# Performance work log

Hardware: AMD Instinct MI355X
Metric: run time of the kernel (lower is better)

Reference implementation:

```python
import jax, jax.numpy as jnp
import numpy as np

NUM_HEADS = 8
D_MODEL = 512
HEAD_DIM = D_MODEL // NUM_HEADS


def _conv1x1(x, W, b):
    # Conv1d(kernel_size=1): x [B, Cin, N], W [Cout, Cin], b [Cout] -> [B, Cout, N]
    return jnp.einsum('oi,bin->bon', W, x) + b[None, :, None]


def setup_inputs() -> dict:
    key = jax.random.key(0)
    ks = jax.random.split(key, 12)
    B, D, N, Mlen = 4, D_MODEL, 2048, 2048
    inp = {
        'query': jax.random.normal(ks[0], (B, D, N), dtype=jnp.float32),
        'key':   jax.random.normal(ks[1], (B, D, Mlen), dtype=jnp.float32),
        'value': jax.random.normal(ks[2], (B, D, Mlen), dtype=jnp.float32),
        'M':     jnp.ones((B, N, Mlen), dtype=jnp.int32),
    }
    scale = 0.02
    inp['Wq'] = jax.random.normal(ks[3], (D, D), dtype=jnp.float32) * scale
    inp['bq'] = jnp.zeros((D,), dtype=jnp.float32)
    inp['Wk'] = jax.random.normal(ks[4], (D, D), dtype=jnp.float32) * scale
    inp['bk'] = jnp.zeros((D,), dtype=jnp.float32)
    inp['Wv'] = jax.random.normal(ks[5], (D, D), dtype=jnp.float32) * scale
    inp['bv'] = jnp.zeros((D,), dtype=jnp.float32)
    inp['Wm'] = jax.random.normal(ks[6], (D, D), dtype=jnp.float32) * scale
    inp['bm'] = jnp.zeros((D,), dtype=jnp.float32)
    return inp


def reference(query, key, value, M, Wq, bq, Wk, bk, Wv, bv, Wm, bm):
    B = query.shape[0]
    # 1x1-conv projections, then channel split as [head_dim, heads] (matches torch .view)
    q = _conv1x1(query, Wq, bq).reshape(B, HEAD_DIM, NUM_HEADS, -1)  # [B, d, h, N]
    k = _conv1x1(key,   Wk, bk).reshape(B, HEAD_DIM, NUM_HEADS, -1)  # [B, d, h, M]
    v = _conv1x1(value, Wv, bv).reshape(B, HEAD_DIM, NUM_HEADS, -1)  # [B, d, h, M]
    scores = jnp.einsum('bdhn,bdhm->bhnm', q, k) / jnp.sqrt(jnp.float32(HEAD_DIM))
    # mask: positions with M==0 are disallowed -> fill with -finfo.max
    bad = (1 - M)[:, None, :, :].astype(bool)  # [B, 1, N, M], broadcasts over heads
    scores = jnp.where(bad, -jnp.finfo(scores.dtype).max, scores)
    prob = jax.nn.softmax(scores, axis=-1)  # [B, h, N, M]
    x = jnp.einsum('bhnm,bdhm->bdhn', prob, v)  # [B, d, h, N]
    out = _conv1x1(x.reshape(B, HEAD_DIM * NUM_HEADS, -1), Wm, bm)  # [B, D, N]
    return out
```

## Files before the change

kernel.cpp:

```cpp
#include <hip/hip_runtime.h>

typedef __attribute__((ext_vector_type(8))) short s8v;
typedef __attribute__((ext_vector_type(4))) float f4v;
typedef _Float16 h8 __attribute__((ext_vector_type(8)));
typedef unsigned short u16;
typedef unsigned long long u64;

#define DM 512
#define NH 8
#define HD 64
#define BB 4
#define NN 2048

extern "C" __device__ float __ocml_native_exp2_f32(float);
__device__ __forceinline__ float fexp2(float x){ return __ocml_native_exp2_f32(x); }

__device__ __forceinline__ float bf2f(u16 x){ return __uint_as_float(((unsigned)x)<<16); }
__device__ __forceinline__ u16 f2bf(float f){
  unsigned u = __float_as_uint(f);
  u += 0x7FFFu + ((u>>16)&1u);
  return (u16)(u>>16);
}
__device__ __forceinline__ void gl2lds16(const u16* g, u16* l){
  __builtin_amdgcn_global_load_lds((__attribute__((address_space(1))) void*)(g),
                                   (__attribute__((address_space(3))) void*)(l), 16, 0, 0);
}

__global__ __launch_bounds__(256) void k_maskpack(const int* M, u64* bits){
  int tid = threadIdx.x;
  int wv = tid>>6, lane = tid&63;
  size_t w0 = (size_t)blockIdx.x*64 + wv*16;
  #pragma unroll
  for (int it=0; it<16; it++){
    int v = M[(w0+it)*64 + lane];
    u64 bal = __ballot(v == 1);
    if (lane == 0) bits[w0+it] = bal;
  }
}

__global__ void k_prep(const float* Wq, const float* bq, const float* Wk, const float* bk,
                       const float* Wv, const float* bv, const float* Wm,
                       u16* Wp, u16* Wmp, float* bp,
                       const u64* bits, u64* allw){
  int blk = blockIdx.x, tid = threadIdx.x;
  if (blk < 1536){
    int t = blk >> 9, op = blk & 511;
    int srow = ((op & 63) << 3) | (op >> 6);
    const float* W = (t==0) ? Wq : ((t==1) ? Wk : Wv);
    for (int j = tid; j < 512; j += 256)
      Wp[((size_t)t*512 + op)*512 + j] = f2bf(W[(size_t)srow*512 + j]);
  } else if (blk < 2048){
    int o = blk - 1536;
    for (int c = tid; c < 512; c += 256){
      int scol = ((c & 63) << 3) | (c >> 6);
      Wmp[(size_t)o*512 + c] = f2bf(Wm[(size_t)o*512 + scol]);
    }
  } else if (blk == 2048){
    for (int idx = tid; idx < 1536; idx += 256){
      int t = idx >> 9, op = idx & 511;
      const float* bs = (t==0) ? bq : ((t==1) ? bk : bv);
      int srow = ((op & 63) << 3) | (op >> 6);
      bp[idx] = bs[srow];
    }
  } else {
    __shared__ u64 red[256];
    int bnt = blk - 2049;
    int mt = tid & 31, rg = tid >> 5;
    const u64* base = bits + (size_t)bnt*64*32;
    u64 v = ~0ull;
    #pragma unroll
    for (int j=0;j<8;j++) v &= base[(size_t)(rg*8+j)*32 + mt];
    red[tid] = v;
    __syncthreads();
    if (tid < 32){
      u64 a = red[tid];
      #pragma unroll
      for (int g2=1; g2<8; g2++) a &= red[g2*32 + tid];
      allw[(size_t)bnt*32 + tid] = a;
    }
  }
}

__global__ __launch_bounds__(256) void k_transpose(const float* q, const float* k, const float* v, u16* XT){
  __shared__ u16 T[64*72];
  int blk = blockIdx.x, tid = threadIdx.x;
  int rt = blk & 31; blk >>= 5;
  int it = blk & 7;  blk >>= 3;
  int b  = blk & 3;  int t = blk >> 2;
  const float* src = (t==0) ? q : ((t==1) ? k : v);
  src += (size_t)b*DM*NN;
  int i0 = it*64, r0 = rt*64;
  int il = tid>>4, rj = (tid&15)*4;
  #pragma unroll
  for (int p=0;p<4;p++){
    int i = il + p*16;
    float4 vv = *(const float4*)&src[(size_t)(i0+i)*NN + r0 + rj];
    float fv[4] = {vv.x, vv.y, vv.z, vv.w};
    #pragma unroll
    for (int qq=0;qq<4;qq++){
      int r = rj + qq;
      int sr = ((r&3)<<4) | (r>>2);
      T[sr*72 + i] = f2bf(fv[qq]);
    }
  }
  __syncthreads();
  u16* dst = XT + ((size_t)(t*4+b)*NN)*DM;
  int rl = tid>>3, ib = (tid&7)*8;
  #pragma unroll
  for (int p=0;p<2;p++){
    int r = rl + p*32;
    int sr = ((r&3)<<4) | (r>>2);
    s8v vv = *(s8v*)&T[sr*72 + ib];
    *(s8v*)&dst[(size_t)(r0+r)*DM + i0 + ib] = vv;
  }
}

__global__ __launch_bounds__(256) void k_proj(const u16* XT, const u16* Wp, const float* bp,
                                              u16* P, u16* VT){
  __shared__ u16 Al[128*32];
  __shared__ u16 Bl[128*32];
  __shared__ u16 S[128*72];
  int blk = blockIdx.x, tid = threadIdx.x;
  int nt = blk / 192; int mt = blk % 192;
  int tb = mt >> 4;
  int t  = tb >> 2, b = tb & 3;
  int r0 = (mt & 15)*128, o0 = nt*128;
  const u16* Abase = XT + ((size_t)tb*NN + r0)*DM;
  const u16* Bbase = Wp + ((size_t)t*512 + o0)*DM;

  int w = tid>>6, L = tid&63, li = L&15, lq = L>>4;
  int wr = w>>1, wc = w&1;
  int srow = tid>>2;
  int g8   = ((tid&3) ^ ((tid>>3)&3))*8;
  u16* AldsW = &Al[((tid&192))*8];
  u16* BldsW = &Bl[((tid&192))*8];
  int sw = (li>>1)&3;

  f4v acc[4][4];
  #pragma unroll
  for (int a=0;a<4;a++)
    #pragma unroll
    for (int c2=0;c2<4;c2++) acc[a][c2] = (f4v){0.f,0.f,0.f,0.f};

  for (int kk=0; kk<16; kk++){
    int k0 = kk*32;
    __syncthreads();
    #pragma unroll
    for (int c=0;c<2;c++){
      gl2lds16(&Abase[(size_t)(srow + c*64)*DM + k0 + g8], AldsW + c*2048);
      gl2lds16(&Bbase[(size_t)(srow + c*64)*DM + k0 + g8], BldsW + c*2048);
    }
    __syncthreads();
    s8v af[4], bfr[4];
    #pragma unroll
    for (int a=0;a<4;a++){
      int r = wr*64 + a*16 + li;
      af[a] = *(s8v*)&Al[r*32 + ((lq ^ sw))*8];
    }
    #pragma unroll
    for (int c2=0;c2<4;c2++){
      int r = wc*64 + c2*16 + li;
      bfr[c2] = *(s8v*)&Bl[r*32 + ((lq ^ sw))*8];
    }
    #pragma unroll
    for (int a=0;a<4;a++)
      #pragma unroll
      for (int c2=0;c2<4;c2++)
        acc[a][c2] = __builtin_amdgcn_mfma_f32_16x16x32_bf16(af[a], bfr[c2], acc[a][c2], 0, 0, 0);
  }

  if (t < 2){
    float scale = (t==0) ? 0.18033688f : 1.0f;
    #pragma unroll
    for (int p=0;p<2;p++){
      if (wc == p){
        #pragma unroll
        for (int c2=0;c2<4;c2++){
          int cl = c2*16 + li;
          float bias = bp[t*512 + o0 + p*64 + cl];
          #pragma unroll
          for (int a=0;a<4;a++)
            #pragma unroll
            for (int ri=0;ri<4;ri++)
              S[(wr*64 + a*16 + lq*4 + ri)*72 + cl] = f2bf((acc[a][c2][ri] + bias)*scale);
        }
      }
      __syncthreads();
      int row = tid>>1, cb = (tid&1)*32;
      int hh = (o0>>6) + p;
      u16* Pb = P + (((size_t)tb*NH + hh)*NN + r0 + row)*HD + cb;
      #pragma unroll
      for (int c=0;c<4;c++){
        s8v vv = *(s8v*)&S[row*72 + cb + c*8];
        *(s8v*)&Pb[c*8] = vv;
      }
      __syncthreads();
    }
  } else {
    int mp = mt & 15;
    #pragma unroll
    for (int p=0;p<2;p++){
      if (wc == p){
        #pragma unroll
        for (int c2=0;c2<4;c2++){
          int cl = c2*16 + li;
          float bias = bp[2*512 + o0 + p*64 + cl];
          #pragma unroll
          for (int a=0;a<4;a++)
            #pragma unroll
            for (int ri=0;ri<4;ri++){
              _Float16 hh = (_Float16)(acc[a][c2][ri] + bias);
              S[(wr*64 + a*16 + lq*4 + ri)*72 + cl] = *(const u16*)&hh;
            }
        }
      }
      __syncthreads();
      int hh = (o0>>6) + p;
      u16* Vbw = VT + ((size_t)(b*NH + hh)*16 + mp)*8192;
      #pragma unroll
      for (int it2=0; it2<4; it2++){
        int c = tid + it2*256;
        int w2  = c >> 8;
        int d   = (c >> 2) & 63;
        int lq2 = c & 3;
        u16 tmp[8];
        #pragma unroll
        for (int t2=0;t2<8;t2++){
          int ml = ((t2>>2)<<6) + w2*16 + lq2*4 + (t2&3);
          tmp[t2] = S[ml*72 + d];
        }
        *(s8v*)&Vbw[(size_t)w2*2048 + d*32 + lq2*8] = *(s8v*)&tmp[0];
      }
      __syncthreads();
    }
  }
}

__global__ __launch_bounds__(256) void k_flash(const u16* Pq, const u16* VT, const u64* bits,
                                               const u64* allw, u16* Xout){
  __shared__ __align__(16) char smem[18432 + 1024];
  float* Red = (float*)smem;
  float* lsb = (float*)(smem + 18432);

  int blk = blockIdx.x, tid = threadIdx.x;
  int bh = blk & 31; int nt = blk >> 5;
  int b = bh >> 3;
  int n0 = nt*64;
  const size_t TSZ = (size_t)BB*NH*NN*HD;
  const u16* Qb = Pq + ((size_t)bh*NN + n0)*HD;
  const u16* Kb = Pq + TSZ + (size_t)bh*NN*HD;
  const u16* Vb = VT + (size_t)bh*NN*HD;
  const u64* awp = allw + ((size_t)b*32 + nt)*32;

  int w = tid>>6, L = tid&63, li = L&15, lq = L>>4;

  s8v Qf[4][2];
  #pragma unroll
  for (int j=0;j<4;j++)
    #pragma unroll
    for (int h2=0;h2<2;h2++)
      Qf[j][h2] = *(const s8v*)&Qb[(size_t)(j*16+li)*HD + h2*32 + lq*8];

  f4v O[4][4];
  #pragma unroll
  for (int j2=0;j2<4;j2++)
    #pragma unroll
    for (int j=0;j<4;j++) O[j2][j] = (f4v){0.f,0.f,0.f,0.f};
  float ls[4] = {0.f,0.f,0.f,0.f};

  const u16* Krow = Kb + (size_t)(w*16 + li)*HD + lq*8;
  const u16* Vrow = Vb + (size_t)w*2048 + li*32 + lq*8;

  s8v cKA0 = *(const s8v*)&Krow[0];
  s8v cKA1 = *(const s8v*)&Krow[32];
  s8v cKB0 = *(const s8v*)&Krow[4096];
  s8v cKB1 = *(const s8v*)&Krow[4128];

  int mbit = w*16 + lq*4;

  for (int mp=0; mp<16; mp++){
    size_t noff = (size_t)((mp+1)&15)*8192;
    s8v nKA0 = *(const s8v*)&Krow[noff];
    s8v nKA1 = *(const s8v*)&Krow[noff + 32];
    s8v nKB0 = *(const s8v*)&Krow[noff + 4096];
    s8v nKB1 = *(const s8v*)&Krow[noff + 4128];
    size_t voff = (size_t)mp*8192;
    h8 cV[4];
    #pragma unroll
    for (int j2=0;j2<4;j2++) cV[j2] = *(const h8*)&Vrow[voff + j2*512];

    u64 awA = awp[2*mp], awB = awp[2*mp+1];
    h8 Pf[4];
    f4v S[4];

    __builtin_amdgcn_s_setprio(1);
    #pragma unroll
    for (int j=0;j<4;j++){
      f4v c = (f4v){0.f,0.f,0.f,0.f};
      c = __builtin_amdgcn_mfma_f32_16x16x32_bf16(cKA0, Qf[j][0], c, 0, 0, 0);
      c = __builtin_amdgcn_mfma_f32_16x16x32_bf16(cKA1, Qf[j][1], c, 0, 0, 0);
      S[j] = c;
    }
    __builtin_amdgcn_s_setprio(0);
    if (awA == ~0ull){
      #pragma unroll
      for (int j=0;j<4;j++){
        float e0 = fexp2(S[j][0]), e1 = fexp2(S[j][1]);
        float e2 = fexp2(S[j][2]), e3 = fexp2(S[j][3]);
        ls[j] += (e0+e1)+(e2+e3);
        Pf[j][0] = (_Float16)e0; Pf[j][1] = (_Float16)e1;
        Pf[j][2] = (_Float16)e2; Pf[j][3] = (_Float16)e3;
      }
    } else {
      #pragma unroll
      for (int j=0;j<4;j++){
        u64 mw = bits[((size_t)b*NN + n0 + j*16 + li)*32 + 2*mp];
        float e[4];
        #pragma unroll
        for (int r=0;r<4;r++){
          float ev = fexp2(S[j][r]);
          e[r] = ((mw>>(mbit+r)) & 1ull) ? ev : 0.f;
          Pf[j][r] = (_Float16)e[r];
        }
        ls[j] += (e[0]+e[1])+(e[2]+e[3]);
      }
    }

    __builtin_amdgcn_s_setprio(1);
    #pragma unroll
    for (int j=0;j<4;j++){
      f4v c = (f4v){0.f,0.f,0.f,0.f};
      c = __builtin_amdgcn_mfma_f32_16x16x32_bf16(cKB0, Qf[j][0], c, 0, 0, 0);
      c = __builtin_amdgcn_mfma_f32_16x16x32_bf16(cKB1, Qf[j][1], c, 0, 0, 0);
      S[j] = c;
    }
    __builtin_amdgcn_s_setprio(0);
    if (awB == ~0ull){
      #pragma unroll
      for (int j=0;j<4;j++){
        float e0 = fexp2(S[j][0]), e1 = fexp2(S[j][1]);
        float e2 = fexp2(S[j][2]), e3 = fexp2(S[j][3]);
        ls[j] += (e0+e1)+(e2+e3);
        Pf[j][4] = (_Float16)e0; Pf[j][5] = (_Float16)e1;
        Pf[j][6] = (_Float16)e2; Pf[j][7] = (_Float16)e3;
      }
    } else {
      #pragma unroll
      for (int j=0;j<4;j++){
        u64 mw = bits[((size_t)b*NN + n0 + j*16 + li)*32 + 2*mp + 1];
        float e[4];
        #pragma unroll
        for (int r=0;r<4;r++){
          float ev = fexp2(S[j][r]);
          e[r] = ((mw>>(mbit+r)) & 1ull) ? ev : 0.f;
          Pf[j][4+r] = (_Float16)e[r];
        }
        ls[j] += (e[0]+e[1])+(e[2]+e[3]);
      }
    }

    __builtin_amdgcn_s_setprio(1);
    #pragma unroll
    for (int j2=0;j2<4;j2++)
      #pragma unroll
      for (int j=0;j<4;j++)
        O[j2][j] = __builtin_amdgcn_mfma_f32_16x16x32_f16(cV[j2], Pf[j], O[j2][j], 0, 0, 0);
    __builtin_amdgcn_s_setprio(0);

    cKA0 = nKA0; cKA1 = nKA1; cKB0 = nKB0; cKB1 = nKB1;
  }

  #pragma unroll
  for (int j=0;j<4;j++){
    float r = ls[j];
    r += __shfl_xor(r, 16); r += __shfl_xor(r, 32);
    ls[j] = r;
  }
  if (lq == 0){
    #pragma unroll
    for (int j=0;j<4;j++) lsb[w*64 + j*16 + li] = ls[j];
  }
  __syncthreads();

  #pragma unroll
  for (int ph=0; ph<4; ph++){
    if (w == ph){
      #pragma unroll
      for (int j=0;j<4;j++)
        #pragma unroll
        for (int j2=0;j2<4;j2++){
          f4v* p = (f4v*)&Red[(j*16+li)*68 + j2*16 + lq*4];
          if (ph == 0) *p = O[j2][j];
          else { f4v t = *p; t += O[j2][j]; *p = t; }
        }
    }
    __syncthreads();
  }

  int n = tid>>2, d0 = (tid&3)*16;
  float s = lsb[n] + lsb[64+n] + lsb[128+n] + lsb[192+n];
  float inv = (s > 0.f) ? 1.0f/s : 0.f;
  int h = bh & 7;
  u16* Xo = Xout + ((size_t)b*NN + n0 + n)*DM + h*HD + d0;
  u16 tmp[16];
  #pragma unroll
  for (int e2=0;e2<4;e2++){
    f4v vv = *(f4v*)&Red[n*68 + d0 + e2*4];
    #pragma unroll
    for (int q2=0;q2<4;q2++) tmp[e2*4+q2] = f2bf(vv[q2]*inv);
  }
  *(s8v*)&Xo[0] = *(s8v*)&tmp[0];
  *(s8v*)&Xo[8] = *(s8v*)&tmp[8];
}

__global__ __launch_bounds__(256) void k_out(const u16* Wmp, const u16* Xout, const float* bm, float* out){
  __shared__ u16 Al[64*32];
  __shared__ u16 Bl[128*32];
  int blk = blockIdx.x, tid = threadIdx.x;
  int nt = blk & 15; blk >>= 4;
  int ot = blk & 7;  int b = blk >> 3;
  int o0 = ot*64, n0 = nt*128;
  const u16* Abase = Wmp + (size_t)o0*DM;
  const u16* Bbase = Xout + ((size_t)b*NN + n0)*DM;

  int w = tid>>6, L = tid&63, li = L&15, lq = L>>4;
  int wo = w&1, wn = w>>1;
  int srow = tid>>2;
  int g8   = ((tid&3) ^ ((tid>>3)&3))*8;
  u16* AldsW = &Al[((tid&192))*8];
  u16* BldsW = &Bl[((tid&192))*8];
  int sw = (li>>1)&3;

  f4v acc[2][4];
  #pragma unroll
  for (int a=0;a<2;a++)
    #pragma unroll
    for (int c2=0;c2<4;c2++) acc[a][c2] = (f4v){0.f,0.f,0.f,0.f};

  for (int kk=0; kk<16; kk++){
    int k0 = kk*32;
    __syncthreads();
    gl2lds16(&Abase[(size_t)srow*DM + k0 + g8], AldsW);
    #pragma unroll
    for (int c=0;c<2;c++)
      gl2lds16(&Bbase[(size_t)(srow + c*64)*DM + k0 + g8], BldsW + c*2048);
    __syncthreads();
    s8v af[2], bfr[4];
    #pragma unroll
    for (int a=0;a<2;a++){
      int r = wo*32 + a*16 + li;
      af[a] = *(s8v*)&Al[r*32 + ((lq ^ sw))*8];
    }
    #pragma unroll
    for (int c2=0;c2<4;c2++){
      int r = wn*64 + c2*16 + li;
      bfr[c2] = *(s8v*)&Bl[r*32 + ((lq ^ sw))*8];
    }
    #pragma unroll
    for (int a=0;a<2;a++)
      #pragma unroll
      for (int c2=0;c2<4;c2++)
        acc[a][c2] = __builtin_amdgcn_mfma_f32_16x16x32_bf16(af[a], bfr[c2], acc[a][c2], 0, 0, 0);
  }

  #pragma unroll
  for (int a=0;a<2;a++){
    #pragma unroll
    for (int ri=0;ri<4;ri++){
      int o = o0 + wo*32 + a*16 + lq*4 + ri;
      float bias = bm[o];
      float* ob = out + ((size_t)b*DM + o)*NN + n0 + wn*64;
      #pragma unroll
      for (int c2=0;c2<4;c2++)
        ob[c2*16 + li] = acc[a][c2][ri] + bias;
    }
  }
}

extern "C" void kernel_launch(void* const* d_in, const int* in_sizes, int n_in,
                              void* d_out, int out_size, void* d_ws, size_t ws_size,
                              hipStream_t stream){
  const float* q  = (const float*)d_in[0];
  const float* k  = (const float*)d_in[1];
  const float* v  = (const float*)d_in[2];
  const int*   M  = (const int*)d_in[3];
  const float* Wq = (const float*)d_in[4];
  const float* bq = (const float*)d_in[5];
  const float* Wk = (const float*)d_in[6];
  const float* bk = (const float*)d_in[7];
  const float* Wv = (const float*)d_in[8];
  const float* bv = (const float*)d_in[9];
  const float* Wm = (const float*)d_in[10];
  const float* bm = (const float*)d_in[11];

  char* ws = (char*)d_ws;
  u16*   XT   = (u16*)(ws + 0);
  u16*   P    = (u16*)(ws + 25165824);
  u16*   VT   = (u16*)(ws + 41943040);
  u16*   Wp   = (u16*)(ws + 50331648);
  u16*   Wmp  = (u16*)(ws + 51904512);
  float* bp   = (float*)(ws + 52428800);
  u64*   bits = (u64*)(ws + 52434944);
  u16*   Xout = (u16*)(ws + 54532096);
  u64*   allw = (u64*)(ws + 62920704);
  float* out  = (float*)d_out;

  k_maskpack<<<4096, 256, 0, stream>>>(M, bits);
  k_prep<<<2177, 256, 0, stream>>>(Wq, bq, Wk, bk, Wv, bv, Wm, Wp, Wmp, bp, bits, allw);
  k_transpose<<<3072, 256, 0, stream>>>(q, k, v, XT);
  k_proj<<<768, 256, 0, stream>>>(XT, Wp, bp, P, VT);
  k_flash<<<1024, 256, 0, stream>>>(P, VT, bits, allw, Xout);
  k_out<<<512, 256, 0, stream>>>(Wmp, Xout, bm, out);
}
```

Measured before the change: 278.2 us.

## Fuse mask packing, weight prep and transpose into one pre kernel; trim flash registers

Merges the mask-packing, weight/bias prep and input-transpose kernels into a single launch. The mask-block AND reduction is now computed directly from the ballots, so the separate pass over the bits buffer goes away and two launches are saved. In the flash kernel, the cross-iteration K prefetch is removed, the V load moves after the first QK MFMA, and launch bounds request 3 blocks per SM to lower register pressure and raise occupancy. The cost is less explicit latency hiding of the K loads.

```diff
diff --git a/kernel.cpp b/kernel.cpp
--- a/kernel.cpp
+++ b/kernel.cpp
@@ -26,36 +26,55 @@
                                    (__attribute__((address_space(3))) void*)(l), 16, 0, 0);
 }
 
-__global__ __launch_bounds__(256) void k_maskpack(const int* M, u64* bits){
-  int tid = threadIdx.x;
-  int wv = tid>>6, lane = tid&63;
-  size_t w0 = (size_t)blockIdx.x*64 + wv*16;
-  #pragma unroll
-  for (int it=0; it<16; it++){
-    int v = M[(w0+it)*64 + lane];
-    u64 bal = __ballot(v == 1);
-    if (lane == 0) bits[w0+it] = bal;
-  }
-}
-
-__global__ void k_prep(const float* Wq, const float* bq, const float* Wk, const float* bk,
+__global__ __launch_bounds__(256) void k_pre(const int* M, u64* bits, u64* allw,
+                       const float* Wq, const float* bq, const float* Wk, const float* bk,
                        const float* Wv, const float* bv, const float* Wm,
                        u16* Wp, u16* Wmp, float* bp,
-                       const u64* bits, u64* allw){
+                       const float* q, const float* k, const float* v, u16* XT){
+  __shared__ u16 T[64*72];
+  __shared__ u64 red[4][8];
   int blk = blockIdx.x, tid = threadIdx.x;
-  if (blk < 1536){
-    int t = blk >> 9, op = blk & 511;
+
+  if (blk < 512){
+    int mg = blk & 3, bnt = blk >> 2;
+    int wv = tid>>6, lane = tid&63;
+    const int* Mb = M + (size_t)bnt*64*2048 + (size_t)mg*512;
+    u64 acc[8];
+    #pragma unroll
+    for (int j=0;j<8;j++) acc[j] = ~0ull;
+    for (int rr=0; rr<16; rr++){
+      int row = wv*16 + rr;
+      #pragma unroll
+      for (int j=0;j<8;j++){
+        int vv = Mb[(size_t)row*2048 + j*64 + lane];
+        u64 bal = __ballot(vv == 1);
+        acc[j] &= bal;
+        if (lane == 0) bits[((size_t)bnt*64 + row)*32 + mg*8 + j] = bal;
+      }
+    }
+    if (lane == 0){
+      #pragma unroll
+      for (int j=0;j<8;j++) red[wv][j] = acc[j];
+    }
+    __syncthreads();
+    if (tid < 8){
+      u64 a = red[0][tid] & red[1][tid] & red[2][tid] & red[3][tid];
+      allw[(size_t)bnt*32 + mg*8 + tid] = a;
+    }
+  } else if (blk < 2048){
+    int idx = blk - 512;
+    int t = idx >> 9, op = idx & 511;
     int srow = ((op & 63) << 3) | (op >> 6);
     const float* W = (t==0) ? Wq : ((t==1) ? Wk : Wv);
     for (int j = tid; j < 512; j += 256)
       Wp[((size_t)t*512 + op)*512 + j] = f2bf(W[(size_t)srow*512 + j]);
-  } else if (blk < 2048){
-    int o = blk - 1536;
+  } else if (blk < 2560){
+    int o = blk - 2048;
     for (int c = tid; c < 512; c += 256){
       int scol = ((c & 63) << 3) | (c >> 6);
       Wmp[(size_t)o*512 + c] = f2bf(Wm[(size_t)o*512 + scol]);
     }
-  } else if (blk == 2048){
+  } else if (blk == 2560){
     for (int idx = tid; idx < 1536; idx += 256){
       int t = idx >> 9, op = idx & 511;
       const float* bs = (t==0) ? bq : ((t==1) ? bk : bv);
@@ -63,55 +82,36 @@
       bp[idx] = bs[srow];
     }
   } else {
-    __shared__ u64 red[256];
-    int bnt = blk - 2049;
-    int mt = tid & 31, rg = tid >> 5;
-    const u64* base = bits + (size_t)bnt*64*32;
-    u64 v = ~0ull;
-    #pragma unroll
-    for (int j=0;j<8;j++) v &= base[(size_t)(rg*8+j)*32 + mt];
-    red[tid] = v;
-    __syncthreads();
-    if (tid < 32){
-      u64 a = red[tid];
-      #pragma unroll
-      for (int g2=1; g2<8; g2++) a &= red[g2*32 + tid];
-      allw[(size_t)bnt*32 + tid] = a;
-    }
-  }
-}
-
-__global__ __launch_bounds__(256) void k_transpose(const float* q, const float* k, const float* v, u16* XT){
-  __shared__ u16 T[64*72];
-  int blk = blockIdx.x, tid = threadIdx.x;
-  int rt = blk & 31; blk >>= 5;
-  int it = blk & 7;  blk >>= 3;
-  int b  = blk & 3;  int t = blk >> 2;
-  const float* src = (t==0) ? q : ((t==1) ? k : v);
-  src += (size_t)b*DM*NN;
-  int i0 = it*64, r0 = rt*64;
-  int il = tid>>4, rj = (tid&15)*4;
-  #pragma unroll
-  for (int p=0;p<4;p++){
-    int i = il + p*16;
-    float4 vv = *(const float4*)&src[(size_t)(i0+i)*NN + r0 + rj];
-    float fv[4] = {vv.x, vv.y, vv.z, vv.w};
-    #pragma unroll
-    for (int qq=0;qq<4;qq++){
-      int r = rj + qq;
+    int b2 = blk - 2561;
+    int rt = b2 & 31; b2 >>= 5;
+    int it = b2 & 7;  b2 >>= 3;
+    int b  = b2 & 3;  int t = b2 >> 2;
+    const float* src = (t==0) ? q : ((t==1) ? k : v);
+    src += (size_t)b*DM*NN;
+    int i0 = it*64, r0 = rt*64;
+    int il = tid>>4, rj = (tid&15)*4;
+    #pragma unroll
+    for (int p=0;p<4;p++){
+      int i = il + p*16;
+      float4 vv = *(const float4*)&src[(size_t)(i0+i)*NN + r0 + rj];
+      float fv[4] = {vv.x, vv.y, vv.z, vv.w};
+      #pragma unroll
+      for (int qq=0;qq<4;qq++){
+        int r = rj + qq;
+        int sr = ((r&3)<<4) | (r>>2);
+        T[sr*72 + i] = f2bf(fv[qq]);
+      }
+    }
+    __syncthreads();
+    u16* dst = XT + ((size_t)(t*4+b)*NN)*DM;
+    int rl = tid>>3, ib = (tid&7)*8;
+    #pragma unroll
+    for (int p=0;p<2;p++){
+      int r = rl + p*32;
       int sr = ((r&3)<<4) | (r>>2);
-      T[sr*72 + i] = f2bf(fv[qq]);
-    }
-  }
-  __syncthreads();
-  u16* dst = XT + ((size_t)(t*4+b)*NN)*DM;
-  int rl = tid>>3, ib = (tid&7)*8;
-  #pragma unroll
-  for (int p=0;p<2;p++){
-    int r = rl + p*32;
-    int sr = ((r&3)<<4) | (r>>2);
-    s8v vv = *(s8v*)&T[sr*72 + ib];
-    *(s8v*)&dst[(size_t)(r0+r)*DM + i0 + ib] = vv;
+      s8v vv = *(s8v*)&T[sr*72 + ib];
+      *(s8v*)&dst[(size_t)(r0+r)*DM + i0 + ib] = vv;
+    }
   }
 }
 
@@ -236,8 +236,8 @@
   }
 }
 
-__global__ __launch_bounds__(256) void k_flash(const u16* Pq, const u16* VT, const u64* bits,
-                                               const u64* allw, u16* Xout){
+__global__ __launch_bounds__(256, 3) void k_flash(const u16* Pq, const u16* VT, const u64* bits,
+                                                  const u64* allw, u16* Xout){
   __shared__ __align__(16) char smem[18432 + 1024];
   float* Red = (float*)smem;
   float* lsb = (float*)(smem + 18432);
@@ -270,24 +270,16 @@
 
   const u16* Krow = Kb + (size_t)(w*16 + li)*HD + lq*8;
   const u16* Vrow = Vb + (size_t)w*2048 + li*32 + lq*8;
-
-  s8v cKA0 = *(const s8v*)&Krow[0];
-  s8v cKA1 = *(const s8v*)&Krow[32];
-  s8v cKB0 = *(const s8v*)&Krow[4096];
-  s8v cKB1 = *(const s8v*)&Krow[4128];
+  const u64* bitsL = bits + ((size_t)b*NN + n0 + li)*32;
 
   int mbit = w*16 + lq*4;
 
   for (int mp=0; mp<16; mp++){
-    size_t noff = (size_t)((mp+1)&15)*8192;
-    s8v nKA0 = *(const s8v*)&Krow[noff];
-    s8v nKA1 = *(const s8v*)&Krow[noff + 32];
-    s8v nKB0 = *(const s8v*)&Krow[noff + 4096];
-    s8v nKB1 = *(const s8v*)&Krow[noff + 4128];
-    size_t voff = (size_t)mp*8192;
-    h8 cV[4];
-    #pragma unroll
-    for (int j2=0;j2<4;j2++) cV[j2] = *(const h8*)&Vrow[voff + j2*512];
+    size_t off = (size_t)mp*8192;
+    s8v cKA0 = *(const s8v*)&Krow[off];
+    s8v cKA1 = *(const s8v*)&Krow[off + 32];
+    s8v cKB0 = *(const s8v*)&Krow[off + 4096];
+    s8v cKB1 = *(const s8v*)&Krow[off + 4128];
 
     u64 awA = awp[2*mp], awB = awp[2*mp+1];
     h8 Pf[4];
@@ -302,6 +294,11 @@
       S[j] = c;
     }
     __builtin_amdgcn_s_setprio(0);
+
+    h8 cV[4];
+    #pragma unroll
+    for (int j2=0;j2<4;j2++) cV[j2] = *(const h8*)&Vrow[off + j2*512];
+
     if (awA == ~0ull){
       #pragma unroll
       for (int j=0;j<4;j++){
@@ -314,7 +311,7 @@
     } else {
       #pragma unroll
       for (int j=0;j<4;j++){
-        u64 mw = bits[((size_t)b*NN + n0 + j*16 + li)*32 + 2*mp];
+        u64 mw = bitsL[j*512 + 2*mp];
         float e[4];
         #pragma unroll
         for (int r=0;r<4;r++){
@@ -347,7 +344,7 @@
     } else {
       #pragma unroll
       for (int j=0;j<4;j++){
-        u64 mw = bits[((size_t)b*NN + n0 + j*16 + li)*32 + 2*mp + 1];
+        u64 mw = bitsL[j*512 + 2*mp + 1];
         float e[4];
         #pragma unroll
         for (int r=0;r<4;r++){
@@ -366,8 +363,6 @@
       for (int j=0;j<4;j++)
         O[j2][j] = __builtin_amdgcn_mfma_f32_16x16x32_f16(cV[j2], Pf[j], O[j2][j], 0, 0, 0);
     __builtin_amdgcn_s_setprio(0);
-
-    cKA0 = nKA0; cKA1 = nKA1; cKB0 = nKB0; cKB1 = nKB1;
   }
 
   #pragma unroll
@@ -505,9 +500,8 @@
   u64*   allw = (u64*)(ws + 62920704);
   float* out  = (float*)d_out;
 
-  k_maskpack<<<4096, 256, 0, stream>>>(M, bits);
-  k_prep<<<2177, 256, 0, stream>>>(Wq, bq, Wk, bk, Wv, bv, Wm, Wp, Wmp, bp, bits, allw);
-  k_transpose<<<3072, 256, 0, stream>>>(q, k, v, XT);
+  k_pre<<<5633, 256, 0, stream>>>(M, bits, allw, Wq, bq, Wk, bk, Wv, bv, Wm,
+                                  Wp, Wmp, bp, q, k, v, XT);
   k_proj<<<768, 256, 0, stream>>>(XT, Wp, bp, P, VT);
   k_flash<<<1024, 256, 0, stream>>>(P, VT, bits, allw, Xout);
   k_out<<<512, 256, 0, stream>>>(Wmp, Xout, bm, out);
```

Result: slower. 398.5 us (+43.2%).

## Split PV output across waves via LDS exchange of P instead of partial-O reduction

Applied to the files above, without the earlier changes.

Each wave now owns a 16-wide slice of the head dimension for the PV product rather than all 64 dims over its own key slice. Softmax probabilities are shared through double-buffered, XOR-swizzled LDS with a barrier per key block. This shrinks the O accumulator from 16 to 4 tiles and removes the four-phase cross-wave output reduction, which enables a min-blocks hint of 3. In exchange it adds an LDS round trip and a __syncthreads every iteration, and it drops the K prefetch and the s_setprio hints.

```diff
diff --git a/kernel.cpp b/kernel.cpp
--- a/kernel.cpp
+++ b/kernel.cpp
@@ -236,11 +236,12 @@
   }
 }
 
-__global__ __launch_bounds__(256) void k_flash(const u16* Pq, const u16* VT, const u64* bits,
-                                               const u64* allw, u16* Xout){
-  __shared__ __align__(16) char smem[18432 + 1024];
+__global__ __launch_bounds__(256, 3) void k_flash(const u16* Pq, const u16* VT, const u64* bits,
+                                                  const u64* allw, u16* Xout){
+  __shared__ __align__(16) char smem[33792];
+  u16*   PL  = (u16*)smem;
+  float* lsb = (float*)(smem + 32768);
   float* Red = (float*)smem;
-  float* lsb = (float*)(smem + 18432);
 
   int blk = blockIdx.x, tid = threadIdx.x;
   int bh = blk & 31; int nt = blk >> 5;
@@ -261,39 +262,31 @@
     for (int h2=0;h2<2;h2++)
       Qf[j][h2] = *(const s8v*)&Qb[(size_t)(j*16+li)*HD + h2*32 + lq*8];
 
-  f4v O[4][4];
-  #pragma unroll
-  for (int j2=0;j2<4;j2++)
-    #pragma unroll
-    for (int j=0;j<4;j++) O[j2][j] = (f4v){0.f,0.f,0.f,0.f};
+  f4v O[4];
+  #pragma unroll
+  for (int j=0;j<4;j++) O[j] = (f4v){0.f,0.f,0.f,0.f};
   float ls[4] = {0.f,0.f,0.f,0.f};
 
   const u16* Krow = Kb + (size_t)(w*16 + li)*HD + lq*8;
-  const u16* Vrow = Vb + (size_t)w*2048 + li*32 + lq*8;
-
-  s8v cKA0 = *(const s8v*)&Krow[0];
-  s8v cKA1 = *(const s8v*)&Krow[32];
-  s8v cKB0 = *(const s8v*)&Krow[4096];
-  s8v cKB1 = *(const s8v*)&Krow[4128];
+  const u16* Vrow = Vb + (size_t)w*512 + li*32 + lq*8;
 
   int mbit = w*16 + lq*4;
+  int wr16 = ((w<<2)+lq)^li;
 
   for (int mp=0; mp<16; mp++){
-    size_t noff = (size_t)((mp+1)&15)*8192;
-    s8v nKA0 = *(const s8v*)&Krow[noff];
-    s8v nKA1 = *(const s8v*)&Krow[noff + 32];
-    s8v nKB0 = *(const s8v*)&Krow[noff + 4096];
-    s8v nKB1 = *(const s8v*)&Krow[noff + 4128];
-    size_t voff = (size_t)mp*8192;
+    size_t off = (size_t)mp*8192;
+    s8v cKA0 = *(const s8v*)&Krow[off];
+    s8v cKA1 = *(const s8v*)&Krow[off + 32];
+    s8v cKB0 = *(const s8v*)&Krow[off + 4096];
+    s8v cKB1 = *(const s8v*)&Krow[off + 4128];
     h8 cV[4];
     #pragma unroll
-    for (int j2=0;j2<4;j2++) cV[j2] = *(const h8*)&Vrow[voff + j2*512];
+    for (int ks=0;ks<4;ks++) cV[ks] = *(const h8*)&Vrow[off + ks*2048];
 
     u64 awA = awp[2*mp], awB = awp[2*mp+1];
     h8 Pf[4];
     f4v S[4];
 
-    __builtin_amdgcn_s_setprio(1);
     #pragma unroll
     for (int j=0;j<4;j++){
       f4v c = (f4v){0.f,0.f,0.f,0.f};
@@ -301,7 +294,6 @@
       c = __builtin_amdgcn_mfma_f32_16x16x32_bf16(cKA1, Qf[j][1], c, 0, 0, 0);
       S[j] = c;
     }
-    __builtin_amdgcn_s_setprio(0);
     if (awA == ~0ull){
       #pragma unroll
       for (int j=0;j<4;j++){
@@ -326,7 +318,6 @@
       }
     }
 
-    __builtin_amdgcn_s_setprio(1);
     #pragma unroll
     for (int j=0;j<4;j++){
       f4v c = (f4v){0.f,0.f,0.f,0.f};
@@ -334,7 +325,6 @@
       c = __builtin_amdgcn_mfma_f32_16x16x32_bf16(cKB1, Qf[j][1], c, 0, 0, 0);
       S[j] = c;
     }
-    __builtin_amdgcn_s_setprio(0);
     if (awB == ~0ull){
       #pragma unroll
       for (int j=0;j<4;j++){
@@ -359,15 +349,22 @@
       }
     }
 
-    __builtin_amdgcn_s_setprio(1);
-    #pragma unroll
-    for (int j2=0;j2<4;j2++)
+    u16* PLc = PL + (mp&1)*8192;
+    #pragma unroll
+    for (int j=0;j<4;j++)
+      *(h8*)&PLc[((j*16+li)<<7) + (wr16<<3)] = Pf[j];
+    __syncthreads();
+
+    #pragma unroll
+    for (int ks=0;ks<4;ks++){
+      h8 pf[4];
       #pragma unroll
       for (int j=0;j<4;j++)
-        O[j2][j] = __builtin_amdgcn_mfma_f32_16x16x32_f16(cV[j2], Pf[j], O[j2][j], 0, 0, 0);
-    __builtin_amdgcn_s_setprio(0);
-
-    cKA0 = nKA0; cKA1 = nKA1; cKB0 = nKB0; cKB1 = nKB1;
+        pf[j] = *(const h8*)&PLc[((j*16+li)<<7) + (((((ks<<2)+lq))^li)<<3)];
+      #pragma unroll
+      for (int j=0;j<4;j++)
+        O[j] = __builtin_amdgcn_mfma_f32_16x16x32_f16(cV[ks], pf[j], O[j], 0, 0, 0);
+    }
   }
 
   #pragma unroll
@@ -383,19 +380,9 @@
   __syncthreads();
 
   #pragma unroll
-  for (int ph=0; ph<4; ph++){
-    if (w == ph){
-      #pragma unroll
-      for (int j=0;j<4;j++)
-        #pragma unroll
-        for (int j2=0;j2<4;j2++){
-          f4v* p = (f4v*)&Red[(j*16+li)*68 + j2*16 + lq*4];
-          if (ph == 0) *p = O[j2][j];
-          else { f4v t = *p; t += O[j2][j]; *p = t; }
-        }
-    }
-    __syncthreads();
-  }
+  for (int j=0;j<4;j++)
+    *(f4v*)&Red[(j*16+li)*68 + w*16 + lq*4] = O[j];
+  __syncthreads();
 
   int n = tid>>2, d0 = (tid&3)*16;
   float s = lsb[n] + lsb[64+n] + lsb[128+n] + lsb[192+n];
```

Result: slower. 285.7 us (+2.7%).
